# Kernel tuning notes

Hardware: AMD Instinct MI355X
Metric: run time of the kernel (lower is better)

Reference implementation:

```python
import jax, jax.numpy as jnp
import numpy as np

BN_EPS = 1e-5
K = 3  # kernel size


def conv2d(x, w, b, pad):
    y = jax.lax.conv_general_dilated(
        x, w, window_strides=(1, 1), padding=[(pad, pad), (pad, pad)],
        dimension_numbers=('NCHW', 'OIHW', 'NCHW'))
    return y + b[None, :, None, None]


def setup_inputs() -> dict:
    key = jax.random.key(0)
    ks = jax.random.split(key, 4)
    B, C, H, W, O = 8, 256, 64, 64, 256
    x = jax.random.normal(ks[0], (B, C, H, W), dtype=jnp.float32)
    # offset/mask conv: 3*dg*k*k = 27 out channels; small init -> small offsets
    w_off = jax.random.normal(ks[1], (27, C, K, K), dtype=jnp.float32) * 0.01
    b_off = jnp.zeros((27,), dtype=jnp.float32)
    # main deformable conv weight/bias
    w = jax.random.normal(ks[2], (O, C, K, K), dtype=jnp.float32) * 0.05
    b = jnp.zeros((O,), dtype=jnp.float32)
    # BatchNorm (inference) params / running stats
    gamma = jnp.ones((O,), dtype=jnp.float32)
    beta = jnp.zeros((O,), dtype=jnp.float32)
    run_mean = jnp.zeros((O,), dtype=jnp.float32)
    run_var = jnp.ones((O,), dtype=jnp.float32)
    return {"x": x, "w_off": w_off, "b_off": b_off, "w": w, "b": b,
            "gamma": gamma, "beta": beta, "run_mean": run_mean, "run_var": run_var}


def _dcn_bn_relu(x, w_off, b_off, w, b, gamma, beta, run_mean, run_var):
    B, C, H, W = x.shape
    KK = K * K
    # offset + modulation mask (DCNv2): channels [0:9]=dy, [9:18]=dx, [18:27]=mask
    om = conv2d(x, w_off, b_off, pad=1)            # [B, 27, H, W]
    dy, dx = om[:, :KK], om[:, KK:2 * KK]          # [B, 9, H, W]
    mod = jax.nn.sigmoid(om[:, 2 * KK:])           # [B, 9, H, W]

    ky, kx = jnp.meshgrid(jnp.arange(K), jnp.arange(K), indexing='ij')
    # base sampling grid: out pixel + dilation*(k - center), padding=1
    base_y = jnp.arange(H, dtype=jnp.float32)[None, :, None] - 1.0 + ky.reshape(KK, 1, 1)
    base_x = jnp.arange(W, dtype=jnp.float32)[None, None, :] - 1.0 + kx.reshape(KK, 1, 1)
    py = base_y[None] + dy                          # [B, 9, H, W]
    px = base_x[None] + dx

    y0 = jnp.floor(py); x0 = jnp.floor(px)
    fy = py - y0; fx = px - x0
    y0 = y0.astype(jnp.int32); x0 = x0.astype(jnp.int32)

    x_flat = x.reshape(B, C, H * W)
    gather = jax.vmap(lambda xf, idx: xf[:, idx])   # ([C,HW],[9,H,W]) -> [C,9,H,W]

    def corner(yi, xi, wgt):
        valid = (yi >= 0) & (yi < H) & (xi >= 0) & (xi < W)
        idx = jnp.clip(yi, 0, H - 1) * W + jnp.clip(xi, 0, W - 1)
        val = gather(x_flat, idx)                   # [B, C, 9, H, W]
        return val * (wgt * valid.astype(wgt.dtype))[:, None]

    sampled = (corner(y0,     x0,     (1 - fy) * (1 - fx))
               + corner(y0,     x0 + 1, (1 - fy) * fx)
               + corner(y0 + 1, x0,     fy * (1 - fx))
               + corner(y0 + 1, x0 + 1, fy * fx))    # [B, C, 9, H, W]
    sampled = sampled * mod[:, None]                 # modulation

    O = w.shape[0]
    out = jnp.einsum('bckhw,ock->bohw', sampled, w.reshape(O, C, KK))
    out = out + b[None, :, None, None]

    # BatchNorm2d (inference) + ReLU
    inv = gamma / jnp.sqrt(run_var + BN_EPS)
    out = out * inv[None, :, None, None] + (beta - run_mean * inv)[None, :, None, None]
    return jax.nn.relu(out)


def reference(x, w_off, b_off, w, b, gamma, beta, run_mean, run_var):
    return _dcn_bn_relu(x, w_off, b_off, w, b, gamma, beta, run_mean, run_var)
```

## Files before the change

### kernel.cpp

```cpp
#include <hip/hip_runtime.h>
#include <math.h>

#define B_   8
#define C_   256
#define H_   64
#define W_   64
#define O_   256
#define KK_  9
#define CK_  2304
#define HW_  4096
#define BN_EPS 1e-5f

typedef __bf16 bf16x8 __attribute__((ext_vector_type(8)));
typedef float  f32x4  __attribute__((ext_vector_type(4)));

static __device__ __forceinline__ unsigned short f2bf(float f) {
    unsigned int u = __float_as_uint(f);
    unsigned int r = (u + 0x7fffu + ((u >> 16) & 1u)) >> 16;
    return (unsigned short)r;
}
static __device__ __forceinline__ unsigned int packbf2(float lo, float hi) {
    unsigned int ul = __float_as_uint(lo) + 0x8000u;
    unsigned int uh = __float_as_uint(hi) + 0x8000u;
    return __builtin_amdgcn_perm(uh, ul, 0x07060302u);
}

__global__ __launch_bounds__(256) void prep_kernel(
    const float* __restrict__ x, const float* __restrict__ w,
    const float* __restrict__ w_off,
    float* __restrict__ xF, unsigned short* __restrict__ wKf,
    unsigned short* __restrict__ wof)
{
    int blk = blockIdx.x;
    if (blk < 2048) {
        __shared__ float tile[64][65];
        const int b   = blk & 7;
        const int ct  = (blk >> 3) & 3;
        const int hwt = blk >> 5;
        const int c0  = ct * 64, hw0 = hwt * 64;
        const int tl  = threadIdx.x & 63, tg = threadIdx.x >> 6;
#pragma unroll
        for (int r = 0; r < 16; ++r) {
            int c_l = tg + r * 4;
            tile[c_l][tl] = x[((size_t)(b * C_ + c0 + c_l)) * HW_ + hw0 + tl];
        }
        __syncthreads();
#pragma unroll
        for (int r = 0; r < 16; ++r) {
            int hw_l = tg + r * 4;
            xF[((size_t)(b * HW_ + hw0 + hw_l)) * C_ + c0 + tl] = tile[tl][hw_l];
        }
    } else if (blk < 2048 + 2304) {
        int idx = (blk - 2048) * 256 + threadIdx.x;
        int o   = idx / CK_;
        int rem = idx - o * CK_;
        int c   = rem / 9;
        int tap = rem - c * 9;
        int NT  = o >> 4, n16 = o & 15;
        int kap = tap * 256 + c;
        int KC  = kap >> 5, kr = kap & 31;
        int lane = ((kr >> 3) << 4) | n16, e = kr & 7;
        wKf[((size_t)(NT * 72 + KC) * 64 + lane) * 8 + e] = f2bf(w[idx]);
    } else {
        int idx = (blk - 4352) * 256 + threadIdx.x;
        int NT  = idx / 36864;
        int r   = idx - NT * 36864;
        int KC  = r >> 9;
        int r2  = r & 511;
        int lane = r2 >> 3, e = r2 & 7;
        int n16 = lane & 15, q = lane >> 4;
        int o   = NT * 16 + n16;
        int kap = KC * 32 + q * 8 + e;
        int tap = kap >> 8, c = kap & 255;
        wof[idx] = (o < 27) ? f2bf(w_off[(o * C_ + c) * KK_ + tap])
                            : (unsigned short)0;
    }
}

__global__ __launch_bounds__(512, 4) void dcn_fused_kernel(
    const float* __restrict__ xF, const unsigned short* __restrict__ wKf,
    const unsigned short* __restrict__ wof, const float* __restrict__ b_off,
    const float* __restrict__ bias, const float* __restrict__ gamma,
    const float* __restrict__ beta, const float* __restrict__ rmean,
    const float* __restrict__ rvar, float* __restrict__ out)
{
    __shared__ __align__(16) unsigned char smem[74528];
    unsigned short* rowbuf = (unsigned short*)smem;
    float4*         wgtv   = (float4*)smem;
    int4*           idxv   = (int4*)(smem + 9216);
    typedef float OmbT[27][64];
    OmbT& omb = *(OmbT*)(smem + 34848);
    typedef unsigned short AbufT[8][4][64][8];
    AbufT& Abuf = *(AbufT*)(smem + 41760);

    const int blk = blockIdx.x;
    const int b = blk & 7, h = blk >> 3;
    const int tid = threadIdx.x, lane = tid & 63, wv = tid >> 6;
    const int m16 = lane & 15, q = lane >> 4;

    if (tid < 33) {
        *(uint4*)&rowbuf[tid * 8] = make_uint4(0u, 0u, 0u, 0u);
    } else if (tid >= 256 && tid < 289) {
        *(uint4*)&rowbuf[65 * 264 + (tid - 256) * 8] = make_uint4(0u, 0u, 0u, 0u);
    }

    const int mi_a = wv & 3, nj_a = wv >> 2;
    f32x4 oacc = {0.f, 0.f, 0.f, 0.f};
    const uint4* wof4 = (const uint4*)wof;

    for (int r = 0; r < 3; ++r) {
        const int hh = h - 1 + r;
        const bool vr = (hh >= 0) && (hh < H_);
        __syncthreads();
        if (vr) {
            const float* src = xF + ((size_t)(b * HW_ + hh * W_)) * C_;
#pragma unroll
            for (int i = 0; i < 4; ++i) {
                const int idx8 = i * 512 + tid;
                f32x4 v0 = *(const f32x4*)(src + idx8 * 8);
                f32x4 v1 = *(const f32x4*)(src + idx8 * 8 + 4);
                uint4 pk;
                pk.x = packbf2(v0[0], v0[1]);
                pk.y = packbf2(v0[2], v0[3]);
                pk.z = packbf2(v1[0], v1[1]);
                pk.w = packbf2(v1[2], v1[3]);
                const int px = idx8 >> 5, c8 = (idx8 & 31) * 8;
                *(uint4*)&rowbuf[(px + 1) * 264 + c8] = pk;
            }
        }
        __syncthreads();
        if (vr) {
#pragma unroll
            for (int s = 0; s < 3; ++s) {
                const unsigned short* arow = &rowbuf[(mi_a * 16 + m16 + s) * 264 + q * 8];
#pragma unroll
                for (int cc = 0; cc < 8; ++cc) {
                    bf16x8 a = *(const bf16x8*)&arow[cc * 32];
                    uint4 braw = wof4[(size_t)(nj_a * 72 + (r * 3 + s) * 8 + cc) * 64 + lane];
                    oacc = __builtin_amdgcn_mfma_f32_16x16x32_bf16(
                        a, __builtin_bit_cast(bf16x8, braw), oacc, 0, 0, 0);
                }
            }
        }
    }
    {
        const int t = nj_a * 16 + m16;
        if (t < 27) {
            const float bo = b_off[t];
            float s0 = oacc[0] + bo, s1 = oacc[1] + bo,
                  s2 = oacc[2] + bo, s3 = oacc[3] + bo;
            if (t >= 18) {
                s0 = 1.f / (1.f + expf(-s0));
                s1 = 1.f / (1.f + expf(-s1));
                s2 = 1.f / (1.f + expf(-s2));
                s3 = 1.f / (1.f + expf(-s3));
            }
            float4 rr; rr.x = s0; rr.y = s1; rr.z = s2; rr.w = s3;
            *(float4*)&omb[t][mi_a * 16 + q * 4] = rr;
        }
    }
    __syncthreads();

    for (int i = tid; i < 576; i += 512) {
        int p = i / 9, t = i - p * 9;
        float dy = omb[t][p];
        float dx = omb[t + 9][p];
        float md = omb[t + 18][p];
        float py = (float)(h - 1 + t / 3) + dy;
        float px = (float)(p - 1 + t % 3) + dx;
        float y0f = floorf(py), x0f = floorf(px);
        int   y0 = (int)y0f,    x0 = (int)x0f;
        float fy = py - y0f,    fx = px - x0f;
        int y0c = min(max(y0,     0), H_ - 1), y1c = min(max(y0 + 1, 0), H_ - 1);
        int x0c = min(max(x0,     0), W_ - 1), x1c = min(max(x0 + 1, 0), W_ - 1);
        float vy0 = (y0     >= 0 && y0     < H_) ? 1.f : 0.f;
        float vy1 = (y0 + 1 >= 0 && y0 + 1 < H_) ? 1.f : 0.f;
        float vx0 = (x0     >= 0 && x0     < W_) ? 1.f : 0.f;
        float vx1 = (x0 + 1 >= 0 && x0 + 1 < W_) ? 1.f : 0.f;
        wgtv[i] = make_float4((1.f - fy) * (1.f - fx) * vy0 * vx0 * md,
                              (1.f - fy) * fx         * vy0 * vx1 * md,
                              fy         * (1.f - fx) * vy1 * vx0 * md,
                              fy         * fx         * vy1 * vx1 * md);
        const int rowb = (b * HW_) * (C_ * 4);
        idxv[i] = make_int4(rowb + (y0c * W_ + x0c) * (C_ * 4),
                            rowb + (y0c * W_ + x1c) * (C_ * 4),
                            rowb + (y1c * W_ + x0c) * (C_ * 4),
                            rowb + (y1c * W_ + x1c) * (C_ * 4));
    }
    __syncthreads();

    f32x4 acc[4][2];
#pragma unroll
    for (int mi = 0; mi < 4; ++mi)
#pragma unroll
        for (int nj = 0; nj < 2; ++nj)
#pragma unroll
            for (int r = 0; r < 4; ++r) acc[mi][nj][r] = 0.f;

    const uint4* wKf4 = (const uint4*)wKf;
    const char*  xFb  = (const char*)xF;

    const int s_cc = lane >> 3;
    const int s_q2 = (lane >> 1) & 3;
    const int s_j0 = (lane & 1) * 4;
    const int s_xr = (s_q2 << 1) ^ s_cc;
    const int s_mi = wv >> 1;
    const int s_pb = (wv & 1) * 8;
    const int loff = lane * 16;

    const int r_row = lane ^ ((lane >> 4) << 1);

    for (int tap = 0; tap < 9; ++tap) {
        uint2 pk[8];
#pragma unroll
        for (int pp = 0; pp < 8; ++pp) {
            const int p = wv * 8 + pp;
            const int4   iq = idxv[p * 9 + tap];
            const float4 wq = wgtv[p * 9 + tap];
            f32x4 c0 = *(const f32x4*)(xFb + iq.x + loff);
            f32x4 c1 = *(const f32x4*)(xFb + iq.y + loff);
            f32x4 c2 = *(const f32x4*)(xFb + iq.z + loff);
            f32x4 c3 = *(const f32x4*)(xFb + iq.w + loff);
            f32x4 g = c0 * wq.x + c1 * wq.y + c2 * wq.z + c3 * wq.w;
            pk[pp].x = packbf2(g[0], g[1]);
            pk[pp].y = packbf2(g[2], g[3]);
        }

        __syncthreads();
#pragma unroll
        for (int pp = 0; pp < 8; ++pp) {
            const int P   = s_pb + pp;
            const int row = (P ^ s_xr) | (s_q2 << 4);
            *(uint2*)&Abuf[s_cc][s_mi][row][s_j0] = pk[pp];
        }
        __syncthreads();

#pragma unroll
        for (int cc = 0; cc < 8; ++cc) {
            const int KC = tap * 8 + cc;
            const int rr = r_row ^ cc;
            uint4 braw[2];
#pragma unroll
            for (int nj = 0; nj < 2; ++nj)
                braw[nj] = wKf4[(size_t)((wv * 2 + nj) * 72 + KC) * 64 + lane];
            bf16x8 a[4];
#pragma unroll
            for (int mi = 0; mi < 4; ++mi)
                a[mi] = *(const bf16x8*)&Abuf[cc][mi][rr][0];
#pragma unroll
            for (int nj = 0; nj < 2; ++nj) {
                bf16x8 bb = __builtin_bit_cast(bf16x8, braw[nj]);
#pragma unroll
                for (int mi = 0; mi < 4; ++mi)
                    acc[mi][nj] = __builtin_amdgcn_mfma_f32_16x16x32_bf16(
                        a[mi], bb, acc[mi][nj], 0, 0, 0);
            }
        }
    }

#pragma unroll
    for (int nj = 0; nj < 2; ++nj) {
        const int o = wv * 32 + nj * 16 + (lane & 15);
        const float inv = gamma[o] * rsqrtf(rvar[o] + BN_EPS);
        const float sh  = beta[o] + (bias[o] - rmean[o]) * inv;
        float* ob = out + ((size_t)(b * O_ + o)) * HW_ + h * W_;
#pragma unroll
        for (int mi = 0; mi < 4; ++mi) {
            f32x4 v = acc[mi][nj];
            float4 r;
            r.x = fmaxf(v[0] * inv + sh, 0.f);
            r.y = fmaxf(v[1] * inv + sh, 0.f);
            r.z = fmaxf(v[2] * inv + sh, 0.f);
            r.w = fmaxf(v[3] * inv + sh, 0.f);
            *(float4*)&ob[mi * 16 + (lane >> 4) * 4] = r;
        }
    }
}

extern "C" void kernel_launch(void* const* d_in, const int* in_sizes, int n_in,
                              void* d_out, int out_size, void* d_ws, size_t ws_size,
                              hipStream_t stream) {
    const float* x     = (const float*)d_in[0];
    const float* w_off = (const float*)d_in[1];
    const float* b_off = (const float*)d_in[2];
    const float* w     = (const float*)d_in[3];
    const float* bias  = (const float*)d_in[4];
    const float* gamma = (const float*)d_in[5];
    const float* beta  = (const float*)d_in[6];
    const float* rmean = (const float*)d_in[7];
    const float* rvar  = (const float*)d_in[8];
    float* out = (float*)d_out;

    float*          xF  = (float*)d_ws;
    unsigned short* wKf = (unsigned short*)(xF + 8388608);
    unsigned short* wof = wKf + 589824;

    prep_kernel<<<4640, 256, 0, stream>>>(x, w, w_off, xF, wKf, wof);
    dcn_fused_kernel<<<512, 512, 0, stream>>>(
        xF, wKf, wof, b_off, bias, gamma, beta, rmean, rvar, out);
}
```

Measured before the change: 190.8 us.

## Store transposed input as bf16 and coalesce weight repacking in prep kernel

The prep kernel now writes the channel-last copy of x in bf16 instead of fp32. This halves both the write traffic and the bilinear gather traffic in the fused kernel, and it drops the per-row pack step during the offset conv. Weight and offset-weight repacking now stage coalesced loads through shared memory instead of scattered per-element gathers, and the grid shrinks accordingly. The trade-off is that the bilinear corner values are rounded to bf16 before interpolation, which adds a small precision loss.

```diff
diff --git a/kernel.cpp b/kernel.cpp
--- a/kernel.cpp
+++ b/kernel.cpp
@@ -24,61 +24,97 @@
     unsigned int uh = __float_as_uint(hi) + 0x8000u;
     return __builtin_amdgcn_perm(uh, ul, 0x07060302u);
 }
+static __device__ __forceinline__ float bflo(unsigned int u) {
+    return __uint_as_float(u << 16);
+}
+static __device__ __forceinline__ float bfhi(unsigned int u) {
+    return __uint_as_float(u & 0xffff0000u);
+}
 
 __global__ __launch_bounds__(256) void prep_kernel(
     const float* __restrict__ x, const float* __restrict__ w,
     const float* __restrict__ w_off,
-    float* __restrict__ xF, unsigned short* __restrict__ wKf,
+    unsigned short* __restrict__ xT, unsigned short* __restrict__ wKf,
     unsigned short* __restrict__ wof)
 {
-    int blk = blockIdx.x;
-    if (blk < 2048) {
-        __shared__ float tile[64][65];
-        const int b   = blk & 7;
-        const int ct  = (blk >> 3) & 3;
-        const int hwt = blk >> 5;
-        const int c0  = ct * 64, hw0 = hwt * 64;
-        const int tl  = threadIdx.x & 63, tg = threadIdx.x >> 6;
-#pragma unroll
-        for (int r = 0; r < 16; ++r) {
-            int c_l = tg + r * 4;
-            tile[c_l][tl] = x[((size_t)(b * C_ + c0 + c_l)) * HW_ + hw0 + tl];
-        }
-        __syncthreads();
-#pragma unroll
-        for (int r = 0; r < 16; ++r) {
-            int hw_l = tg + r * 4;
-            xF[((size_t)(b * HW_ + hw0 + hw_l)) * C_ + c0 + tl] = tile[tl][hw_l];
-        }
-    } else if (blk < 2048 + 2304) {
-        int idx = (blk - 2048) * 256 + threadIdx.x;
-        int o   = idx / CK_;
-        int rem = idx - o * CK_;
-        int c   = rem / 9;
-        int tap = rem - c * 9;
-        int NT  = o >> 4, n16 = o & 15;
-        int kap = tap * 256 + c;
-        int KC  = kap >> 5, kr = kap & 31;
-        int lane = ((kr >> 3) << 4) | n16, e = kr & 7;
-        wKf[((size_t)(NT * 72 + KC) * 64 + lane) * 8 + e] = f2bf(w[idx]);
+    __shared__ float tile[64][65];
+    __shared__ float wbuf[4608];
+
+    const int blk = blockIdx.x;
+    const int tid = threadIdx.x, lane = tid & 63, tg = tid >> 6;
+
+    if (blk < 512) {
+        const int b = blk & 7, h = blk >> 3;
+        const int hwb = h * W_;
+#pragma unroll
+        for (int ct = 0; ct < 4; ++ct) {
+            const int c0 = ct * 64;
+#pragma unroll
+            for (int r = 0; r < 16; ++r) {
+                int c_l = tg + r * 4;
+                tile[c_l][lane] = x[((size_t)(b * C_ + c0 + c_l)) * HW_ + hwb + lane];
+            }
+            __syncthreads();
+#pragma unroll
+            for (int it = 0; it < 4; ++it) {
+                const int hw_l = tg * 16 + it * 4 + (lane >> 4);
+                const int c_l4 = (lane & 15) * 4;
+                float v0 = tile[c_l4 + 0][hw_l];
+                float v1 = tile[c_l4 + 1][hw_l];
+                float v2 = tile[c_l4 + 2][hw_l];
+                float v3 = tile[c_l4 + 3][hw_l];
+                uint2 pk;
+                pk.x = packbf2(v0, v1);
+                pk.y = packbf2(v2, v3);
+                *(uint2*)&xT[((size_t)(b * HW_ + hwb + hw_l)) * C_ + c0 + c_l4] = pk;
+            }
+            __syncthreads();
+        }
+    } else if (blk < 640) {
+        const int t2 = blk - 512;
+        const int NT = t2 >> 3, cb = t2 & 7;
+#pragma unroll
+        for (int i = 0; i < 18; ++i) {
+            int j = i * 256 + tid;
+            int o_l = j / 288, rest = j - o_l * 288;
+            wbuf[o_l * 288 + rest] = w[(size_t)(NT * 16 + o_l) * CK_ + cb * 288 + rest];
+        }
+        __syncthreads();
+#pragma unroll
+        for (int i = 0; i < 18; ++i) {
+            int d = i * 256 + tid;
+            int tap = d >> 9, r5 = d & 511;
+            int ln = r5 >> 3, e = r5 & 7;
+            int n16 = ln & 15, q = ln >> 4;
+            float val = wbuf[n16 * 288 + (q * 8 + e) * 9 + tap];
+            wKf[((size_t)(NT * 72 + tap * 8 + cb) * 64 + ln) * 8 + e] = f2bf(val);
+        }
     } else {
-        int idx = (blk - 4352) * 256 + threadIdx.x;
-        int NT  = idx / 36864;
-        int r   = idx - NT * 36864;
-        int KC  = r >> 9;
-        int r2  = r & 511;
-        int lane = r2 >> 3, e = r2 & 7;
-        int n16 = lane & 15, q = lane >> 4;
-        int o   = NT * 16 + n16;
-        int kap = KC * 32 + q * 8 + e;
-        int tap = kap >> 8, c = kap & 255;
-        wof[idx] = (o < 27) ? f2bf(w_off[(o * C_ + c) * KK_ + tap])
-                            : (unsigned short)0;
+        const int t2 = blk - 640;
+        const int NT = t2 >> 3, cb = t2 & 7;
+#pragma unroll
+        for (int i = 0; i < 18; ++i) {
+            int j = i * 256 + tid;
+            int o_l = j / 288, rest = j - o_l * 288;
+            int o = NT * 16 + o_l;
+            wbuf[o_l * 288 + rest] =
+                (o < 27) ? w_off[(size_t)o * CK_ + cb * 288 + rest] : 0.f;
+        }
+        __syncthreads();
+#pragma unroll
+        for (int i = 0; i < 18; ++i) {
+            int d = i * 256 + tid;
+            int tap = d >> 9, r5 = d & 511;
+            int ln = r5 >> 3, e = r5 & 7;
+            int n16 = ln & 15, q = ln >> 4;
+            float val = wbuf[n16 * 288 + (q * 8 + e) * 9 + tap];
+            wof[((size_t)(NT * 72 + tap * 8 + cb) * 64 + ln) * 8 + e] = f2bf(val);
+        }
     }
 }
 
 __global__ __launch_bounds__(512, 4) void dcn_fused_kernel(
-    const float* __restrict__ xF, const unsigned short* __restrict__ wKf,
+    const unsigned short* __restrict__ xT, const unsigned short* __restrict__ wKf,
     const unsigned short* __restrict__ wof, const float* __restrict__ b_off,
     const float* __restrict__ bias, const float* __restrict__ gamma,
     const float* __restrict__ beta, const float* __restrict__ rmean,
@@ -113,19 +149,13 @@
         const bool vr = (hh >= 0) && (hh < H_);
         __syncthreads();
         if (vr) {
-            const float* src = xF + ((size_t)(b * HW_ + hh * W_)) * C_;
+            const uint4* src = (const uint4*)&xT[((size_t)(b * HW_ + hh * W_)) * C_];
 #pragma unroll
             for (int i = 0; i < 4; ++i) {
                 const int idx8 = i * 512 + tid;
-                f32x4 v0 = *(const f32x4*)(src + idx8 * 8);
-                f32x4 v1 = *(const f32x4*)(src + idx8 * 8 + 4);
-                uint4 pk;
-                pk.x = packbf2(v0[0], v0[1]);
-                pk.y = packbf2(v0[2], v0[3]);
-                pk.z = packbf2(v1[0], v1[1]);
-                pk.w = packbf2(v1[2], v1[3]);
+                uint4 v = src[idx8];
                 const int px = idx8 >> 5, c8 = (idx8 & 31) * 8;
-                *(uint4*)&rowbuf[(px + 1) * 264 + c8] = pk;
+                *(uint4*)&rowbuf[(px + 1) * 264 + c8] = v;
             }
         }
         __syncthreads();
@@ -181,11 +211,11 @@
                               (1.f - fy) * fx         * vy0 * vx1 * md,
                               fy         * (1.f - fx) * vy1 * vx0 * md,
                               fy         * fx         * vy1 * vx1 * md);
-        const int rowb = (b * HW_) * (C_ * 4);
-        idxv[i] = make_int4(rowb + (y0c * W_ + x0c) * (C_ * 4),
-                            rowb + (y0c * W_ + x1c) * (C_ * 4),
-                            rowb + (y1c * W_ + x0c) * (C_ * 4),
-                            rowb + (y1c * W_ + x1c) * (C_ * 4));
+        const int rowb = (b * HW_) * (C_ * 2);
+        idxv[i] = make_int4(rowb + (y0c * W_ + x0c) * (C_ * 2),
+                            rowb + (y0c * W_ + x1c) * (C_ * 2),
+                            rowb + (y1c * W_ + x0c) * (C_ * 2),
+                            rowb + (y1c * W_ + x1c) * (C_ * 2));
     }
     __syncthreads();
 
@@ -198,7 +228,7 @@
             for (int r = 0; r < 4; ++r) acc[mi][nj][r] = 0.f;
 
     const uint4* wKf4 = (const uint4*)wKf;
-    const char*  xFb  = (const char*)xF;
+    const char*  xTb  = (const char*)xT;
 
     const int s_cc = lane >> 3;
     const int s_q2 = (lane >> 1) & 3;
@@ -206,7 +236,7 @@
     const int s_xr = (s_q2 << 1) ^ s_cc;
     const int s_mi = wv >> 1;
     const int s_pb = (wv & 1) * 8;
-    const int loff = lane * 16;
+    const int loff = lane * 8;
 
     const int r_row = lane ^ ((lane >> 4) << 1);
 
@@ -217,13 +247,16 @@
             const int p = wv * 8 + pp;
             const int4   iq = idxv[p * 9 + tap];
             const float4 wq = wgtv[p * 9 + tap];
-            f32x4 c0 = *(const f32x4*)(xFb + iq.x + loff);
-            f32x4 c1 = *(const f32x4*)(xFb + iq.y + loff);
-            f32x4 c2 = *(const f32x4*)(xFb + iq.z + loff);
-            f32x4 c3 = *(const f32x4*)(xFb + iq.w + loff);
-            f32x4 g = c0 * wq.x + c1 * wq.y + c2 * wq.z + c3 * wq.w;
-            pk[pp].x = packbf2(g[0], g[1]);
-            pk[pp].y = packbf2(g[2], g[3]);
+            const uint2 k0 = *(const uint2*)(xTb + iq.x + loff);
+            const uint2 k1 = *(const uint2*)(xTb + iq.y + loff);
+            const uint2 k2 = *(const uint2*)(xTb + iq.z + loff);
+            const uint2 k3 = *(const uint2*)(xTb + iq.w + loff);
+            float g0 = wq.x*bflo(k0.x) + wq.y*bflo(k1.x) + wq.z*bflo(k2.x) + wq.w*bflo(k3.x);
+            float g1 = wq.x*bfhi(k0.x) + wq.y*bfhi(k1.x) + wq.z*bfhi(k2.x) + wq.w*bfhi(k3.x);
+            float g2 = wq.x*bflo(k0.y) + wq.y*bflo(k1.y) + wq.z*bflo(k2.y) + wq.w*bflo(k3.y);
+            float g3 = wq.x*bfhi(k0.y) + wq.y*bfhi(k1.y) + wq.z*bfhi(k2.y) + wq.w*bfhi(k3.y);
+            pk[pp].x = packbf2(g0, g1);
+            pk[pp].y = packbf2(g2, g3);
         }
 
         __syncthreads();
@@ -291,11 +324,11 @@
     const float* rvar  = (const float*)d_in[8];
     float* out = (float*)d_out;
 
-    float*          xF  = (float*)d_ws;
-    unsigned short* wKf = (unsigned short*)(xF + 8388608);
+    unsigned short* xT  = (unsigned short*)d_ws;
+    unsigned short* wKf = xT + 8388608;
     unsigned short* wof = wKf + 589824;
 
-    prep_kernel<<<4640, 256, 0, stream>>>(x, w, w_off, xF, wKf, wof);
+    prep_kernel<<<656, 256, 0, stream>>>(x, w, w_off, xT, wKf, wof);
     dcn_fused_kernel<<<512, 512, 0, stream>>>(
-        xF, wKf, wof, b_off, bias, gamma, beta, rmean, rvar, out);
-}
+        xT, wKf, wof, b_off, bias, gamma, beta, rmean, rvar, out);
+}
```

Measured after the change: 183.1 us. -4.1%, faster.
